# Kernel tuning notes

Measured on AMD Instinct MI355X. Metric: run time of the kernel, lower is better.

The kernel has to match this reference:

```python
import jax, jax.numpy as jnp
import numpy as np

B, M, D, O = 64, 4096, 128, 16


def setup_inputs() -> dict:
    key = jax.random.key(0)
    k1, k2, k3, k4 = jax.random.split(key, 4)
    glorot_w = float(np.sqrt(6.0 / (D + D)))
    glorot_v = float(np.sqrt(6.0 / (2 * D + 1)))
    return {
        "x1": jax.random.normal(k1, (B, D), dtype=jnp.float32),
        "x2": jax.random.normal(k2, (B, M, D), dtype=jnp.float32),
        "W": jax.random.uniform(k3, (O, D, D), minval=-glorot_w, maxval=glorot_w, dtype=jnp.float32),
        "V": jax.random.uniform(k4, (O, 2 * D, 1), minval=-glorot_v, maxval=glorot_v, dtype=jnp.float32),
        "bias": jnp.zeros((O,), dtype=jnp.float32),
    }


def reference(x1, x2, W, V, bias):
    d = x1.shape[1]
    # Bilinear term: x1 . W[o] . x2^T for every output slice o -> [B, M, O]
    s1 = jnp.einsum('bd,odk,bmk->bmo', x1, W, x2)
    # Linear term: V[o]^T concat(x1_tiled, x2). Split V into the x1 part and x2 part.
    v1 = V[:, :d, 0]   # [O, D]
    v2 = V[:, d:, 0]   # [O, D]
    s2 = jnp.einsum('bd,od->bo', x1, v1)[:, None, :] + jnp.einsum('bmd,od->bmo', x2, v2)
    out = jax.nn.relu(s1 + s2 + bias)  # [B, M, O]
    return out.reshape(-1, out.shape[-1])  # [B*M, O], matches concat of [-1,1] slices
```

## Files before the change

kernel.cpp:

```cpp
#include <hip/hip_runtime.h>

#define B_ 64
#define M_ 4096
#define D_ 128
#define O_ 16

typedef __bf16 bf16x8 __attribute__((ext_vector_type(8)));
typedef float  f32x4  __attribute__((ext_vector_type(4)));

__global__ __launch_bounds__(128) void prep_kernel(
    const float* __restrict__ x1, const float* __restrict__ W,
    const float* __restrict__ V, const float* __restrict__ bias,
    __bf16* __restrict__ ub, float* __restrict__ c)
{
    const int o = blockIdx.x;
    const int b = blockIdx.y;
    const int k = threadIdx.x;
    __shared__ float x1s[D_];
    __shared__ float red[2];
    x1s[k] = x1[b * D_ + k];
    __syncthreads();

    const float* Wo = W + o * D_ * D_;
    float acc = 0.f;
    #pragma unroll 8
    for (int d = 0; d < D_; ++d)
        acc = fmaf(x1s[d], Wo[d * D_ + k], acc);

    const float uval = acc + V[o * 2 * D_ + D_ + k];
    const int e  = k & 7;
    const int g  = (k >> 3) & 3;
    const int kb = k >> 5;
    ub[(size_t)b * 2048 + kb * 512 + g * 128 + o * 8 + e] = (__bf16)uval;

    float p = x1s[k] * V[o * 2 * D_ + k];
    #pragma unroll
    for (int off = 32; off; off >>= 1) p += __shfl_down(p, off, 64);
    if ((k & 63) == 0) red[k >> 6] = p;
    __syncthreads();
    if (k == 0) c[b * O_ + o] = red[0] + red[1] + bias[o];
}

__global__ __launch_bounds__(256) void fused_kernel(
    const float* __restrict__ x2, const __bf16* __restrict__ ub,
    const float* __restrict__ c, float* __restrict__ out)
{
    const int b = blockIdx.y;
    const int t = threadIdx.x;

    __shared__ bf16x8 ubs[256];
    ((float4*)ubs)[t] = ((const float4*)(ub + (size_t)b * 2048))[t];
    __syncthreads();

    const int wave = t >> 6, lane = t & 63;
    const int rc = lane & 15;
    const int g  = lane >> 4;

    bf16x8 bfrag[4];
    #pragma unroll
    for (int kb = 0; kb < 4; ++kb) bfrag[kb] = ubs[kb * 64 + lane];

    const float cv = c[b * O_ + rc];
    const int m_base = blockIdx.x * 256 + wave * 64;

    for (int tile = 0; tile < 4; ++tile) {
        const int m0 = m_base + tile * 16;
        const float4* ap = (const float4*)(x2 + ((size_t)b * M_ + m0 + rc) * D_) + g * 2;

        f32x4 acc = {cv, cv, cv, cv};
        #pragma unroll
        for (int kb = 0; kb < 4; ++kb) {
            float4 a0 = ap[kb * 8];
            float4 a1 = ap[kb * 8 + 1];
            bf16x8 af;
            af[0] = (__bf16)a0.x; af[1] = (__bf16)a0.y;
            af[2] = (__bf16)a0.z; af[3] = (__bf16)a0.w;
            af[4] = (__bf16)a1.x; af[5] = (__bf16)a1.y;
            af[6] = (__bf16)a1.z; af[7] = (__bf16)a1.w;
            acc = __builtin_amdgcn_mfma_f32_16x16x32_bf16(af, bfrag[kb], acc, 0, 0, 0);
        }

        float* op = out + ((size_t)b * M_ + m0) * O_ + rc;
        #pragma unroll
        for (int i = 0; i < 4; ++i)
            op[(g * 4 + i) * O_] = fmaxf(acc[i], 0.f);
    }
}

extern "C" void kernel_launch(void* const* d_in, const int* in_sizes, int n_in,
                              void* d_out, int out_size, void* d_ws, size_t ws_size,
                              hipStream_t stream) {
    const float* x1   = (const float*)d_in[0];
    const float* x2   = (const float*)d_in[1];
    const float* W    = (const float*)d_in[2];
    const float* V    = (const float*)d_in[3];
    const float* bias = (const float*)d_in[4];
    float* out = (float*)d_out;

    __bf16* ubf = (__bf16*)d_ws;
    float*  c   = (float*)((char*)d_ws + (size_t)B_ * 2048 * sizeof(__bf16));

    prep_kernel<<<dim3(O_, B_), 128, 0, stream>>>(x1, W, V, bias, ubf, c);
    fused_kernel<<<dim3(M_ / 256, B_), 256, 0, stream>>>(x2, ubf, c, out);
}
```

Measured before the change: 36.44 us.

## Preload all x2 tiles into registers, halve rows per block, drop LDS staging

The fused kernel now gives each wave 32 rows instead of 64 and issues the global loads for both 16-row tiles before any MFMA work, so more memory requests are in flight per wave. The grid doubles to keep every row covered. The shared-memory copy of the bf16 weight fragments and its barrier are removed, and each lane reads its fragments straight from global memory. The risks are higher register pressure from the 16 float4 preloads and repeated reads of the per-batch weights by twice as many blocks.

```diff
diff --git a/kernel.cpp b/kernel.cpp
--- a/kernel.cpp
+++ b/kernel.cpp
@@ -47,40 +47,47 @@
 {
     const int b = blockIdx.y;
     const int t = threadIdx.x;
-
-    __shared__ bf16x8 ubs[256];
-    ((float4*)ubs)[t] = ((const float4*)(ub + (size_t)b * 2048))[t];
-    __syncthreads();
-
     const int wave = t >> 6, lane = t & 63;
     const int rc = lane & 15;
     const int g  = lane >> 4;
 
+    const bf16x8* uf = (const bf16x8*)(ub + (size_t)b * 2048);
     bf16x8 bfrag[4];
     #pragma unroll
-    for (int kb = 0; kb < 4; ++kb) bfrag[kb] = ubs[kb * 64 + lane];
+    for (int kb = 0; kb < 4; ++kb) bfrag[kb] = uf[kb * 64 + lane];
+    const float cv = c[b * O_ + rc];
 
-    const float cv = c[b * O_ + rc];
-    const int m_base = blockIdx.x * 256 + wave * 64;
+    const int m_base = blockIdx.x * 128 + wave * 32;
+    const float4* ap0 = (const float4*)(x2 + ((size_t)b * M_ + m_base + rc) * D_) + g * 2;
+    const float4* ap1 = ap0 + 16 * (D_ / 4);
 
-    for (int tile = 0; tile < 4; ++tile) {
-        const int m0 = m_base + tile * 16;
-        const float4* ap = (const float4*)(x2 + ((size_t)b * M_ + m0 + rc) * D_) + g * 2;
+    float4 a0[8], a1[8];
+    #pragma unroll
+    for (int kb = 0; kb < 4; ++kb) {
+        a0[kb * 2]     = ap0[kb * 8];
+        a0[kb * 2 + 1] = ap0[kb * 8 + 1];
+    }
+    #pragma unroll
+    for (int kb = 0; kb < 4; ++kb) {
+        a1[kb * 2]     = ap1[kb * 8];
+        a1[kb * 2 + 1] = ap1[kb * 8 + 1];
+    }
 
+    #pragma unroll
+    for (int tt = 0; tt < 2; ++tt) {
+        const float4* av = tt ? a1 : a0;
         f32x4 acc = {cv, cv, cv, cv};
         #pragma unroll
         for (int kb = 0; kb < 4; ++kb) {
-            float4 a0 = ap[kb * 8];
-            float4 a1 = ap[kb * 8 + 1];
+            const float* p0 = (const float*)&av[kb * 2];
             bf16x8 af;
-            af[0] = (__bf16)a0.x; af[1] = (__bf16)a0.y;
-            af[2] = (__bf16)a0.z; af[3] = (__bf16)a0.w;
-            af[4] = (__bf16)a1.x; af[5] = (__bf16)a1.y;
-            af[6] = (__bf16)a1.z; af[7] = (__bf16)a1.w;
+            af[0] = (__bf16)p0[0]; af[1] = (__bf16)p0[1];
+            af[2] = (__bf16)p0[2]; af[3] = (__bf16)p0[3];
+            af[4] = (__bf16)p0[4]; af[5] = (__bf16)p0[5];
+            af[6] = (__bf16)p0[6]; af[7] = (__bf16)p0[7];
             acc = __builtin_amdgcn_mfma_f32_16x16x32_bf16(af, bfrag[kb], acc, 0, 0, 0);
         }
-
-        float* op = out + ((size_t)b * M_ + m0) * O_ + rc;
+        float* op = out + ((size_t)b * M_ + m_base + tt * 16) * O_ + rc;
         #pragma unroll
         for (int i = 0; i < 4; ++i)
             op[(g * 4 + i) * O_] = fmaxf(acc[i], 0.f);
@@ -101,5 +108,5 @@
     float*  c   = (float*)((char*)d_ws + (size_t)B_ * 2048 * sizeof(__bf16));
 
     prep_kernel<<<dim3(O_, B_), 128, 0, stream>>>(x1, W, V, bias, ubf, c);
-    fused_kernel<<<dim3(M_ / 256, B_), 256, 0, stream>>>(x2, ubf, c, out);
+    fused_kernel<<<dim3(M_ / 128, B_), 256, 0, stream>>>(x2, ubf, c, out);
 }
```

New measurement: 34.82 us. 4.4% less time.
